# Performance work log

Hardware: AMD Instinct MI355X
Metric: run time of the kernel (lower is better)

The kernel has to match this reference:

```python
import jax, jax.numpy as jnp
import numpy as np
import math

D_MODEL = 1024
N_HEADS = 16
D_K = D_MODEL // N_HEADS
THRESH = 0.1  # attention probs below this are zeroed


def setup_inputs() -> dict:
    key = jax.random.key(0)
    ks = jax.random.split(key, 9)
    B, S, D = 2, 2048, D_MODEL
    scale = 1.0 / math.sqrt(D)
    x = jax.random.normal(ks[0], (B, S, D), dtype=jnp.float32)
    Wq = jax.random.normal(ks[1], (D, D), dtype=jnp.float32) * scale
    bq = jax.random.normal(ks[2], (D,), dtype=jnp.float32) * 0.01
    Wk = jax.random.normal(ks[3], (D, D), dtype=jnp.float32) * scale
    bk = jax.random.normal(ks[4], (D,), dtype=jnp.float32) * 0.01
    Wv = jax.random.normal(ks[5], (D, D), dtype=jnp.float32) * scale
    bv = jax.random.normal(ks[6], (D,), dtype=jnp.float32) * 0.01
    Wo = jax.random.normal(ks[7], (D, D), dtype=jnp.float32) * scale
    bo = jax.random.normal(ks[8], (D,), dtype=jnp.float32) * 0.01
    return {"x": x, "Wq": Wq, "bq": bq, "Wk": Wk, "bk": bk,
            "Wv": Wv, "bv": bv, "Wo": Wo, "bo": bo}


def _split_heads(t):
    B, S, D = t.shape
    return t.reshape(B, S, N_HEADS, D_K).transpose(0, 2, 1, 3)  # [B,H,S,dk]


def reference(x, Wq, bq, Wk, bk, Wv, bv, Wo, bo):
    # torch nn.Linear: y = x @ W.T + b
    q = _split_heads(x @ Wq.T + bq)
    k = _split_heads(x @ Wk.T + bk)
    v = _split_heads(x @ Wv.T + bv)
    scores = jnp.einsum('bhqd,bhkd->bhqk', q, k) / math.sqrt(D_K)
    probs = jax.nn.softmax(scores, axis=-1)          # full unmasked softmax (returned)
    keep = probs >= THRESH                            # ~low_attention_mask
    probs_model = jnp.where(keep, probs, 0.0)        # masked_fill; dropout is identity in eval
    ctx = jnp.einsum('bhqk,bhkd->bhqd', probs_model, v)
    B, H, S, dk = ctx.shape
    merged = ctx.transpose(0, 2, 1, 3).reshape(B, S, H * dk)
    out = merged @ Wo.T + bo
    attention_sum = probs.sum(axis=1)                # [B,S,S] sum over heads
    attention_mask = keep.astype(jnp.float32).sum(axis=1)  # [B,S,S]
    return (out, attention_sum, attention_mask)
```

## Files before the change

kernel.cpp:

```cpp
#include <hip/hip_runtime.h>

#define SDIM 2048
#define DDIM 1024
#define NH 16
#define DK 64
#define NB 2
#define MROWS (NB * SDIM)
#define MAXEV 65536
#define EXPC 0.18033688011112f
#define L01 -3.3219281f

typedef _Float16 f16x8 __attribute__((ext_vector_type(8)));
typedef _Float16 f16x4 __attribute__((ext_vector_type(4)));
typedef float f32x4 __attribute__((ext_vector_type(4)));

__device__ __forceinline__ void ld_lds16(const _Float16* g, _Float16* l) {
  __builtin_amdgcn_global_load_lds(
      (const __attribute__((address_space(1))) void*)g,
      (__attribute__((address_space(3))) void*)l, 16, 0, 0);
}

__global__ __launch_bounds__(256) void cvt_f16(
    const float* __restrict__ x, const float* __restrict__ wq,
    const float* __restrict__ wk, const float* __restrict__ wv,
    _Float16* __restrict__ xh, _Float16* __restrict__ wqh,
    _Float16* __restrict__ wkh, _Float16* __restrict__ wvh) {
  int i = blockIdx.x * 256 + threadIdx.x;
  const float* src;
  _Float16* dst;
  int off;
  if (i < 1048576) {
    src = x; dst = xh; off = i;
  } else if (i < 1310720) {
    src = wq; dst = wqh; off = i - 1048576;
  } else if (i < 1572864) {
    src = wk; dst = wkh; off = i - 1310720;
  } else {
    src = wv; dst = wvh; off = i - 1572864;
  }
  float4 v = ((const float4*)src)[off];
  f16x4 h;
  h[0] = (_Float16)v.x; h[1] = (_Float16)v.y;
  h[2] = (_Float16)v.z; h[3] = (_Float16)v.w;
  ((f16x4*)dst)[off] = h;
}

__global__ __launch_bounds__(256, 2) void proj_gemm(
    const _Float16* __restrict__ xh, const _Float16* __restrict__ Wqh,
    const _Float16* __restrict__ Wkh, const _Float16* __restrict__ Wvh,
    const float* __restrict__ bq, const float* __restrict__ bk,
    const float* __restrict__ bv, _Float16* __restrict__ Qo,
    _Float16* __restrict__ Ko, float* __restrict__ Vo) {
  __shared__ __align__(16) _Float16 SMEM[16896];
  _Float16* sA = SMEM;
  _Float16* sB = SMEM + 128 * 64;
  const int t = threadIdx.x;
  const int lane = t & 63, wv = t >> 6;
  const int lr = lane & 15, quad = lane >> 4;
  const int wm = wv >> 1, wn = wv & 1;
  const int m0 = blockIdx.y * 128, n0 = blockIdx.x * 128;
  const int z = blockIdx.z;
  const _Float16* Bp = z == 0 ? Wqh : (z == 1 ? Wkh : Wvh);
  const float* bias = z == 0 ? bq : (z == 1 ? bk : bv);

  const int strow = t >> 3;
  const int stchunk = t & 7;
  const int stsrc = (stchunk ^ (strow & 7)) * 8;

  f32x4 acc[4][4];
#pragma unroll
  for (int i = 0; i < 4; ++i)
#pragma unroll
    for (int j = 0; j < 4; ++j) acc[i][j] = (f32x4){0.f, 0.f, 0.f, 0.f};

  for (int k0 = 0; k0 < DDIM; k0 += 64) {
    __syncthreads();
#pragma unroll
    for (int i = 0; i < 4; ++i) {
      const int row = i * 32 + strow;
      ld_lds16(&xh[(size_t)(m0 + row) * DDIM + k0 + stsrc],
               &sA[row * 64 + stchunk * 8]);
      ld_lds16(&Bp[(size_t)(n0 + row) * DDIM + k0 + stsrc],
               &sB[row * 64 + stchunk * 8]);
    }
    __syncthreads();
    f16x8 af[4][2], bf[4][2];
#pragma unroll
    for (int i = 0; i < 4; ++i)
#pragma unroll
      for (int kk = 0; kk < 2; ++kk) {
        const int ph = ((kk * 4 + quad) ^ (lr & 7)) * 8;
        af[i][kk] = *(const f16x8*)&sA[(wm * 64 + i * 16 + lr) * 64 + ph];
        bf[i][kk] = *(const f16x8*)&sB[(wn * 64 + i * 16 + lr) * 64 + ph];
      }
#pragma unroll
    for (int kk = 0; kk < 2; ++kk)
#pragma unroll
      for (int i = 0; i < 4; ++i)
#pragma unroll
        for (int j = 0; j < 4; ++j)
          acc[i][j] = __builtin_amdgcn_mfma_f32_16x16x32_f16(
              af[i][kk], bf[j][kk], acc[i][j], 0, 0, 0);
  }

  const int h0 = n0 >> 6;
  const int bb = m0 >> 11;
  const int s0 = m0 & 2047;
  __syncthreads();
  if (z < 2) {
    _Float16* dst = z == 0 ? Qo : Ko;
    _Float16* Tb = SMEM;
    const float scl = z == 0 ? EXPC : 1.0f;
#pragma unroll 1
    for (int p = 0; p < 2; ++p) {
      if (wm == p) {
#pragma unroll
        for (int j = 0; j < 4; ++j) {
          const int ng = wn * 64 + j * 16 + lr;
          const float bvv = bias[n0 + ng];
#pragma unroll
          for (int i = 0; i < 4; ++i)
#pragma unroll
            for (int r = 0; r < 4; ++r) {
              const int row = i * 16 + quad * 4 + r;
              Tb[row * 136 + ng] = (_Float16)((acc[i][j][r] + bvv) * scl);
            }
        }
      }
      __syncthreads();
      const int srow = t >> 4, scc = t & 15;
#pragma unroll
      for (int ii = 0; ii < 4; ++ii) {
        const int row = ii * 16 + srow;
        const int s = s0 + p * 64 + row;
        const int h = h0 + (scc >> 3);
        const int d = (scc & 7) * 8;
        f16x8 v = *(const f16x8*)&Tb[row * 136 + scc * 8];
        *(f16x8*)&dst[((size_t)(bb * NH + h) * SDIM + s) * DK + d] = v;
      }
      __syncthreads();
    }
  } else {
    float* Tb = (float*)SMEM;
#pragma unroll 1
    for (int p = 0; p < 2; ++p) {
      if (wm == p) {
#pragma unroll
        for (int j = 0; j < 4; ++j) {
          const int ng = wn * 64 + j * 16 + lr;
          const float bvv = bias[n0 + ng];
#pragma unroll
          for (int i = 0; i < 4; ++i)
#pragma unroll
            for (int r = 0; r < 4; ++r) {
              const int row = i * 16 + quad * 4 + r;
              Tb[row * 132 + ng] = acc[i][j][r] + bvv;
            }
        }
      }
      __syncthreads();
      const int srow = t >> 5, scc = t & 31;
#pragma unroll
      for (int ii = 0; ii < 8; ++ii) {
        const int row = ii * 8 + srow;
        const int s = s0 + p * 64 + row;
        const int h = h0 + (scc >> 4);
        const int d = (scc & 15) * 4;
        float4 v = *(const float4*)&Tb[row * 132 + scc * 4];
        *(float4*)&Vo[((size_t)(bb * NH + h) * SDIM + s) * DK + d] = v;
      }
      __syncthreads();
    }
  }
}

__global__ __launch_bounds__(256, 3) void attn_denom(
    const _Float16* __restrict__ Q, const _Float16* __restrict__ K,
    float* __restrict__ laOut) {
  __shared__ __align__(16) _Float16 KS[3 * 8192];
  const int t = threadIdx.x;
  const int lane = t & 63, wave = t >> 6;
  const int quad = lane >> 4, lr = lane & 15;
  const int id = blockIdx.x;
  const int xcd = id & 7, inner = id >> 3;
  const int bh = xcd * 4 + (inner >> 5);
  const int q0 = (inner & 31) * 64;
  const _Float16* Qh = Q + (size_t)bh * SDIM * DK;
  const _Float16* Kh = K + (size_t)bh * SDIM * DK;
  const size_t qoff = (size_t)(q0 + wave * 16 + lr) * DK + quad * 8;
  const f16x8 aq0 = *(const f16x8*)&Qh[qoff];
  const f16x8 aq1 = *(const f16x8*)&Qh[qoff + 32];
  const int strow = t >> 3, stchunk = t & 7;
  const int stsrc = (stchunk ^ (strow & 7)) * 8;
  const int ph0 = (quad ^ (lr & 7)) * 8;
  const int ph1 = ((4 + quad) ^ (lr & 7)) * 8;

#define STAGE_DN(KP, BUF)                                                  \
  {                                                                        \
    _Pragma("unroll") for (int i = 0; i < 4; ++i)                          \
        ld_lds16(&(KP)[(size_t)(i * 32 + strow) * DK + stsrc],             \
                 &(BUF)[(i * 32 + strow) * 64 + stchunk * 8]);             \
  }

#define COMPUTE_DN(BUF)                                                   \
  _Pragma("unroll") for (int c = 0; c < 8; ++c) {                         \
    f16x8 b0 = *(const f16x8*)&(BUF)[(c * 16 + lr) * 64 + ph0];           \
    f16x8 b1 = *(const f16x8*)&(BUF)[(c * 16 + lr) * 64 + ph1];           \
    f32x4 acc = {0.f, 0.f, 0.f, 0.f};                                     \
    acc = __builtin_amdgcn_mfma_f32_16x16x32_f16(aq0, b0, acc, 0, 0, 0);  \
    acc = __builtin_amdgcn_mfma_f32_16x16x32_f16(aq1, b1, acc, 0, 0, 0);  \
    _Pragma("unroll") for (int r = 0; r < 4; ++r)                         \
        dsum[r] += __builtin_amdgcn_exp2f(acc[r]);                        \
  }

  float dsum[4] = {0.f, 0.f, 0.f, 0.f};
  const _Float16* kp = Kh;
  STAGE_DN(kp, KS);
  kp += 128 * DK;
  int cb = 0;
#pragma unroll 1
  for (int kt = 0; kt < 16; ++kt) {
    const int nb_ = cb == 2 ? 0 : cb + 1;
    if (kt + 1 < 16) {
      STAGE_DN(kp, KS + nb_ * 8192);
      kp += 128 * DK;
    }
    asm volatile("" ::: "memory");
    if (kt + 1 < 16)
      asm volatile("s_waitcnt vmcnt(4)" ::: "memory");
    else
      asm volatile("s_waitcnt vmcnt(0)" ::: "memory");
    __builtin_amdgcn_s_barrier();
    asm volatile("" ::: "memory");
    __builtin_amdgcn_s_setprio(1);
    COMPUTE_DN(KS + cb * 8192);
    __builtin_amdgcn_s_setprio(0);
    cb = nb_;
  }
#pragma unroll
  for (int m = 1; m < 16; m <<= 1)
#pragma unroll
    for (int r = 0; r < 4; ++r)
      dsum[r] += __shfl_xor(dsum[r], m, 64);
  if (lr == 0) {
#pragma unroll
    for (int r = 0; r < 4; ++r)
      laOut[(size_t)bh * SDIM + q0 + wave * 16 + quad * 4 + r] =
          -__builtin_amdgcn_logf(dsum[r]);
  }
#undef STAGE_DN
#undef COMPUTE_DN
}

__global__ __launch_bounds__(256, 3) void attn_pass2(
    const _Float16* __restrict__ Q, const _Float16* __restrict__ K,
    const float* __restrict__ la, float* __restrict__ attSum,
    float* __restrict__ attMask, float4* __restrict__ ev,
    int* __restrict__ ecnt) {
  __shared__ __align__(16) _Float16 KS[3 * 8192];
  float* Tbuf = (float*)KS;
  const int t = threadIdx.x;
  const int lane = t & 63, wave = t >> 6;
  const int quad = lane >> 4, lr = lane & 15;
  const int id = blockIdx.x;
  const int xcd = id & 7, inner = id >> 3;
  const int b = xcd >> 2;
  const int q0 = (((xcd >> 1) & 1) * 16 + (inner >> 4)) * 64;
  const int k0 = ((xcd & 1) * 16 + (inner & 15)) * 64;
  const int strow = t >> 3, stchunk = t & 7;
  const int stsrc = (stchunk ^ (strow & 7)) * 8;
  const int ph0 = (quad ^ (lr & 7)) * 8;
  const int ph1 = ((4 + quad) ^ (lr & 7)) * 8;

  const size_t qbase = ((size_t)(b * NH) * SDIM + q0 + wave * 16 + lr) * DK;
  const size_t dbase = (size_t)(b * NH) * SDIM + q0 + wave * 16 + quad * 4;
  const size_t hstep = (size_t)SDIM * DK;

  float asum[4][4] = {};
  float mx01 = -1e30f, mx23 = -1e30f;

  f16x8 a0c[2], a1c[2], a0n[2], a1n[2];
  float4 lavc[2], lavn[2];

#define STAGE2(KP, BUF)                                                      \
  {                                                                          \
    _Pragma("unroll") for (int hh = 0; hh < 2; ++hh) {                       \
      const _Float16* Kpp = (KP) + (size_t)hh * hstep;                       \
      _Pragma("unroll") for (int i = 0; i < 2; ++i)                          \
          ld_lds16(&Kpp[(size_t)(i * 32 + strow) * DK + stsrc],              \
                   &(BUF)[hh * 4096 + (i * 32 + strow) * 64 + stchunk * 8]); \
    }                                                                        \
  }

#define LOADQ2(QP, LAP, A0, A1, LV)                                          \
  {                                                                          \
    _Pragma("unroll") for (int hh = 0; hh < 2; ++hh) {                       \
      const _Float16* qpp = (QP) + (size_t)hh * hstep;                       \
      A0[hh] = *(const f16x8*)&qpp[quad * 8];                                \
      A1[hh] = *(const f16x8*)&qpp[32 + quad * 8];                           \
      LV[hh] = *(const float4*)&(LAP)[(size_t)hh * SDIM];                    \
    }                                                                        \
  }

#define COMPUTE2(BUF, A0, A1, LV)                                            \
  _Pragma("unroll") for (int hh = 0; hh < 2; ++hh) {                         \
    const _Float16* Ksh = &(BUF)[hh * 4096];                                 \
    const f32x4 cinit = {LV[hh].x, LV[hh].y, LV[hh].z, LV[hh].w};            \
    _Pragma("unroll") for (int c = 0; c < 4; ++c) {                          \
      f16x8 b0 = *(const f16x8*)&Ksh[(c * 16 + lr) * 64 + ph0];              \
      f16x8 b1 = *(const f16x8*)&Ksh[(c * 16 + lr) * 64 + ph1];              \
      f32x4 acc = cinit;                  \
      acc = __builtin_amdgcn_mfma_f32_16x16x32_f16(A0[hh], b0, acc, 0, 0, 0);\
      acc = __builtin_amdgcn_mfma_f32_16x16x32_f16(A1[hh], b1, acc, 0, 0, 0);\
      mx01 = fmaxf(fmaxf(acc[0], acc[1]), mx01);                 \
      mx23 = fmaxf(fmaxf(acc[2], acc[3]), mx23);                             \
      asum[c][0] += __builtin_amdgcn_exp2f(acc[0]);                          \
      asum[c][1] += __builtin_amdgcn_exp2f(acc[1]);                          \
      asum[c][2] += __builtin_amdgcn_exp2f(acc[2]);                          \
      asum[c][3] += __builtin_amdgcn_exp2f(acc[3]);                          \
    }                                                                        \
  }

  const _Float16* kp = K + (size_t)(b * NH) * hstep + (size_t)k0 * DK;
  const _Float16* qp = Q + qbase;
  const float* lap = la + dbase;
  STAGE2(kp, KS);
  LOADQ2(qp, lap, a0c, a1c, lavc);
  kp += 2 * hstep; qp += 2 * hstep; lap += 2 * SDIM;
  int cb = 0;
#pragma unroll 1
  for (int s = 0; s < 8; ++s) {
    const int nb_ = cb == 2 ? 0 : cb + 1;
    if (s + 1 < 8) {
      STAGE2(kp, KS + nb_ * 8192);
      LOADQ2(qp, lap, a0n, a1n, lavn);
      kp += 2 * hstep; qp += 2 * hstep; lap += 2 * SDIM;
    }
    asm volatile("" ::: "memory");
    if (s + 1 < 8)
      asm volatile("s_waitcnt vmcnt(10)" ::: "memory");
    else
      asm volatile("s_waitcnt vmcnt(0)" ::: "memory");
    __builtin_amdgcn_s_barrier();
    asm volatile("" ::: "memory");
    __builtin_amdgcn_s_setprio(1);
    COMPUTE2(KS + cb * 8192, a0c, a1c, lavc);
    __builtin_amdgcn_s_setprio(0);
    if (s + 1 < 8) {
#pragma unroll
      for (int hh = 0; hh < 2; ++hh) {
        a0c[hh] = a0n[hh]; a1c[hh] = a1n[hh]; lavc[hh] = lavn[hh];
      }
    }
    cb = nb_;
  }
#undef STAGE2
#undef LOADQ2
#undef COMPUTE2

  const float mx = fmaxf(mx01, mx23);
  if (__any(mx >= L01)) {
    float amask[4][4] = {};
#pragma unroll 1
    for (int h = 0; h < NH; ++h) {
      const _Float16* Kp =
          K + (size_t)(b * NH + h) * hstep + (size_t)k0 * DK;
      const size_t ho = (size_t)h * hstep;
      const f16x8 aq0 = *(const f16x8*)&Q[qbase + ho + quad * 8];
      const f16x8 aq1 = *(const f16x8*)&Q[qbase + ho + 32 + quad * 8];
      const float4 l4 = *(const float4*)&la[dbase + (size_t)h * SDIM];
      const float lar[4] = {l4.x, l4.y, l4.z, l4.w};
#pragma unroll 1
      for (int c = 0; c < 4; ++c) {
        const f16x8 b0 = *(const f16x8*)&Kp[(c * 16 + lr) * DK + quad * 8];
        const f16x8 b1 = *(const f16x8*)&Kp[(c * 16 + lr) * DK + 32 + quad * 8];
        f32x4 acc = {0.f, 0.f, 0.f, 0.f};
        acc = __builtin_amdgcn_mfma_f32_16x16x32_f16(aq0, b0, acc, 0, 0, 0);
        acc = __builtin_amdgcn_mfma_f32_16x16x32_f16(aq1, b1, acc, 0, 0, 0);
#pragma unroll 1
        for (int r = 0; r < 4; ++r) {
          const float p = __builtin_amdgcn_exp2f(acc[r] + lar[r]);
          if (p >= 0.1f) {
            amask[c][r] += 1.0f;
            int idx = atomicAdd(ecnt, 1);
            if (idx < MAXEV)
              ev[idx] = make_float4(
                  __int_as_float(b * NH + h),
                  __int_as_float(q0 + wave * 16 + quad * 4 + r),
                  __int_as_float(k0 + c * 16 + lr), p);
          }
        }
      }
    }
#pragma unroll
    for (int c = 0; c < 4; ++c)
#pragma unroll
      for (int r = 0; r < 4; ++r)
        if (amask[c][r] != 0.0f) {
          const size_t row = (size_t)(b * SDIM) + q0 + wave * 16 + quad * 4 + r;
          attMask[row * SDIM + k0 + c * 16 + lr] = amask[c][r];
        }
  }
  const int g8 = t >> 3;
  const int l8 = (t & 7) * 4;
  __syncthreads();
#pragma unroll
  for (int c = 0; c < 4; ++c)
#pragma unroll
    for (int r = 0; r < 4; ++r)
      Tbuf[(wave * 16 + quad * 4 + r) * 68 + c * 16 + lr] = asum[c][r];
  __syncthreads();
#pragma unroll
  for (int p = 0; p < 2; ++p)
#pragma unroll
    for (int qh = 0; qh < 2; ++qh) {
      const int row = p * 32 + g8, col = qh * 32 + l8;
      f32x4 v = *(const f32x4*)&Tbuf[row * 68 + col];
      __builtin_nontemporal_store(
          v, (f32x4*)&attSum[((size_t)(b * SDIM) + q0 + row) * SDIM + k0 + col]);
    }
}

__global__ __launch_bounds__(64) void apply_events(
    const float4* __restrict__ ev, const int* __restrict__ ecnt,
    const float* __restrict__ V, float* __restrict__ merged,
    int* __restrict__ flags) {
  int n = *ecnt;
  if (n > MAXEV) n = MAXEV;
  const int d = threadIdx.x;
  for (int e = blockIdx.x; e < n; e += gridDim.x) {
    float4 r = ev[e];
    int bh = __float_as_int(r.x);
    int q = __float_as_int(r.y);
    int kc = __float_as_int(r.z);
    float p = r.w;
    int b = bh >> 4, h = bh & 15;
    atomicAdd(&merged[((size_t)(b * SDIM + q)) * DDIM + h * DK + d],
              p * V[((size_t)bh * SDIM + kc) * DK + d]);
    if (d == 0) flags[b * SDIM + q] = 1;
  }
}

__global__ __launch_bounds__(256) void out_gemm(const float* __restrict__ A,
                                                const float* __restrict__ W,
                                                const float* __restrict__ bias,
                                                float* __restrict__ out,
                                                const int* __restrict__ flags) {
  __shared__ float As[16][68];
  __shared__ float Ws[16][68];
  __shared__ int anyF;
  const int t = threadIdx.x;
  const int tx = t & 15, ty = t >> 4;
  const int m0 = blockIdx.y * 64;
  const int n0 = blockIdx.x * 64;
  if (t == 0) anyF = 0;
  __syncthreads();
  if (t < 64 && flags[m0 + t]) anyF = 1;
  __syncthreads();
  const int nb = n0 + tx * 4;
  const float4 bv = *(const float4*)&bias[nb];
  if (!anyF) {
#pragma unroll
    for (int r = 0; r < 4; ++r)
      *(float4*)&out[(size_t)(m0 + ty * 4 + r) * DDIM + nb] = bv;
    return;
  }
  const int lr = t >> 2;
  const int lc = (t & 3) * 4;
  float acc[4][4] = {};
  for (int k0 = 0; k0 < DDIM; k0 += 16) {
    __syncthreads();
    float4 av = *(const float4*)&A[(size_t)(m0 + lr) * DDIM + k0 + lc];
    float4 wv = *(const float4*)&W[(size_t)(n0 + lr) * DDIM + k0 + lc];
    As[lc + 0][lr] = av.x; As[lc + 1][lr] = av.y;
    As[lc + 2][lr] = av.z; As[lc + 3][lr] = av.w;
    Ws[lc + 0][lr] = wv.x; Ws[lc + 1][lr] = wv.y;
    Ws[lc + 2][lr] = wv.z; Ws[lc + 3][lr] = wv.w;
    __syncthreads();
#pragma unroll
    for (int kk = 0; kk < 16; ++kk) {
      float4 a4 = *(const float4*)&As[kk][ty * 4];
      float4 b4 = *(const float4*)&Ws[kk][tx * 4];
      const float a[4] = {a4.x, a4.y, a4.z, a4.w};
      const float b[4] = {b4.x, b4.y, b4.z, b4.w};
#pragma unroll
      for (int r = 0; r < 4; ++r)
#pragma unroll
        for (int c = 0; c < 4; ++c)
          acc[r][c] = fmaf(a[r], b[c], acc[r][c]);
    }
  }
#pragma unroll
  for (int r = 0; r < 4; ++r) {
    float4 o;
    o.x = acc[r][0] + bv.x;
    o.y = acc[r][1] + bv.y;
    o.z = acc[r][2] + bv.z;
    o.w = acc[r][3] + bv.w;
    *(float4*)&out[(size_t)(m0 + ty * 4 + r) * DDIM + nb] = o;
  }
}

extern "C" void kernel_launch(void* const* d_in, const int* in_sizes, int n_in,
                              void* d_out, int out_size, void* d_ws,
                              size_t ws_size, hipStream_t stream) {
  const float* x = (const float*)d_in[0];
  const float* Wq = (const float*)d_in[1];
  const float* bq = (const float*)d_in[2];
  const float* Wk = (const float*)d_in[3];
  const float* bk = (const float*)d_in[4];
  const float* Wv = (const float*)d_in[5];
  const float* bv = (const float*)d_in[6];
  const float* Wo = (const float*)d_in[7];
  const float* bo = (const float*)d_in[8];

  float* out = (float*)d_out;
  float* attSum = out + (size_t)MROWS * DDIM;
  float* attMask = attSum + (size_t)NB * SDIM * SDIM;

  char* ws = (char*)d_ws;
  const size_t bigF = (size_t)MROWS * DDIM * sizeof(float);
  const size_t bigH = (size_t)MROWS * DDIM * sizeof(_Float16);
  const size_t wH = (size_t)DDIM * DDIM * sizeof(_Float16);
  float* merged = (float*)ws;    ws += bigF;
  int* flags = (int*)ws;         ws += (size_t)MROWS * sizeof(int);
  int* ecnt = (int*)ws;          ws += 16;
  const size_t zeroSpan = bigF + (size_t)MROWS * sizeof(int) + 16;
  _Float16* Qh = (_Float16*)ws;  ws += bigH;
  _Float16* Kh = (_Float16*)ws;  ws += bigH;
  float* V = (float*)ws;         ws += bigF;
  _Float16* xh = (_Float16*)ws;  ws += bigH;
  _Float16* Wqh = (_Float16*)ws; ws += wH;
  _Float16* Wkh = (_Float16*)ws; ws += wH;
  _Float16* Wvh = (_Float16*)ws; ws += wH;
  float* laBuf = (float*)ws;     ws += (size_t)NB * NH * SDIM * sizeof(float);
  float4* ev = (float4*)ws;      ws += (size_t)MAXEV * sizeof(float4);

  hipMemsetAsync(merged, 0, zeroSpan, stream);
  hipMemsetAsync(attMask, 0, (size_t)NB * SDIM * SDIM * sizeof(float), stream);

  dim3 blk(256);
  cvt_f16<<<dim3(7168), blk, 0, stream>>>(x, Wq, Wk, Wv, xh, Wqh, Wkh, Wvh);
  proj_gemm<<<dim3(8, 32, 3), blk, 0, stream>>>(xh, Wqh, Wkh, Wvh, bq, bk, bv,
                                                Qh, Kh, V);
  attn_denom<<<dim3(1024), blk, 0, stream>>>(Qh, Kh, laBuf);
  attn_pass2<<<dim3(2048), blk, 0, stream>>>(Qh, Kh, laBuf, attSum,
                                             attMask, ev, ecnt);
  apply_events<<<dim3(256), dim3(64), 0, stream>>>(ev, ecnt, V, merged, flags);
  out_gemm<<<dim3(16, 64), blk, 0, stream>>>(merged, Wo, bo, out, flags);
}
```

Before: 244.6 us.

## Pipeline attn_pass2 per head with 4-slot LDS ring to raise occupancy

The score-sum pass now stages one head's K tile per step into a 4-slot ring buffer with prefetch distance two, instead of two heads per step in a 3-slot buffer. This cuts LDS use from 48KB to 32KB and the register footprint of the Q/la prefetch, so launch bounds go from 3 to 4 blocks per CU. The cost is twice as many barrier-separated steps, each doing less work, and tighter hand-written vmcnt accounting. The smaller LDS array is also shared with a later Tbuf scratch, which must still fit.

```diff
diff --git a/kernel.cpp b/kernel.cpp
--- a/kernel.cpp
+++ b/kernel.cpp
@@ -252,12 +252,12 @@
 #undef COMPUTE_DN
 }
 
-__global__ __launch_bounds__(256, 3) void attn_pass2(
+__global__ __launch_bounds__(256, 4) void attn_pass2(
     const _Float16* __restrict__ Q, const _Float16* __restrict__ K,
     const float* __restrict__ la, float* __restrict__ attSum,
     float* __restrict__ attMask, float4* __restrict__ ev,
     int* __restrict__ ecnt) {
-  __shared__ __align__(16) _Float16 KS[3 * 8192];
+  __shared__ __align__(16) _Float16 KS[4 * 4096];
   float* Tbuf = (float*)KS;
   const int t = threadIdx.x;
   const int lane = t & 63, wave = t >> 6;
@@ -279,39 +279,32 @@
   float asum[4][4] = {};
   float mx01 = -1e30f, mx23 = -1e30f;
 
-  f16x8 a0c[2], a1c[2], a0n[2], a1n[2];
-  float4 lavc[2], lavn[2];
-
-#define STAGE2(KP, BUF)                                                      \
+  f16x8 a0c, a1c, a0n, a1n;
+  float4 lavc, lavn;
+
+#define STAGE1(KP, BUF)                                                      \
   {                                                                          \
-    _Pragma("unroll") for (int hh = 0; hh < 2; ++hh) {                       \
-      const _Float16* Kpp = (KP) + (size_t)hh * hstep;                       \
-      _Pragma("unroll") for (int i = 0; i < 2; ++i)                          \
-          ld_lds16(&Kpp[(size_t)(i * 32 + strow) * DK + stsrc],              \
-                   &(BUF)[hh * 4096 + (i * 32 + strow) * 64 + stchunk * 8]); \
-    }                                                                        \
-  }
-
-#define LOADQ2(QP, LAP, A0, A1, LV)                                          \
+    _Pragma("unroll") for (int i = 0; i < 2; ++i)                            \
+        ld_lds16(&(KP)[(size_t)(i * 32 + strow) * DK + stsrc],               \
+                 &(BUF)[(i * 32 + strow) * 64 + stchunk * 8]);               \
+  }
+
+#define LOADQ1(QP, LAP, A0, A1, LV)                                          \
   {                                                                          \
-    _Pragma("unroll") for (int hh = 0; hh < 2; ++hh) {                       \
-      const _Float16* qpp = (QP) + (size_t)hh * hstep;                       \
-      A0[hh] = *(const f16x8*)&qpp[quad * 8];                                \
-      A1[hh] = *(const f16x8*)&qpp[32 + quad * 8];                           \
-      LV[hh] = *(const float4*)&(LAP)[(size_t)hh * SDIM];                    \
-    }                                                                        \
-  }
-
-#define COMPUTE2(BUF, A0, A1, LV)                                            \
-  _Pragma("unroll") for (int hh = 0; hh < 2; ++hh) {                         \
-    const _Float16* Ksh = &(BUF)[hh * 4096];                                 \
-    const f32x4 cinit = {LV[hh].x, LV[hh].y, LV[hh].z, LV[hh].w};            \
+    A0 = *(const f16x8*)&(QP)[quad * 8];                                     \
+    A1 = *(const f16x8*)&(QP)[32 + quad * 8];                                \
+    LV = *(const float4*)(LAP);                                              \
+  }
+
+#define COMPUTE1(BUF, A0, A1, LV)                                            \
+  {                                                                          \
+    const f32x4 cinit = {LV.x, LV.y, LV.z, LV.w};                            \
     _Pragma("unroll") for (int c = 0; c < 4; ++c) {                          \
-      f16x8 b0 = *(const f16x8*)&Ksh[(c * 16 + lr) * 64 + ph0];              \
-      f16x8 b1 = *(const f16x8*)&Ksh[(c * 16 + lr) * 64 + ph1];              \
+      f16x8 b0 = *(const f16x8*)&(BUF)[(c * 16 + lr) * 64 + ph0];            \
+      f16x8 b1 = *(const f16x8*)&(BUF)[(c * 16 + lr) * 64 + ph1];            \
       f32x4 acc = cinit;                  \
-      acc = __builtin_amdgcn_mfma_f32_16x16x32_f16(A0[hh], b0, acc, 0, 0, 0);\
-      acc = __builtin_amdgcn_mfma_f32_16x16x32_f16(A1[hh], b1, acc, 0, 0, 0);\
+      acc = __builtin_amdgcn_mfma_f32_16x16x32_f16(A0, b0, acc, 0, 0, 0);    \
+      acc = __builtin_amdgcn_mfma_f32_16x16x32_f16(A1, b1, acc, 0, 0, 0);    \
       mx01 = fmaxf(fmaxf(acc[0], acc[1]), mx01);                 \
       mx23 = fmaxf(fmaxf(acc[2], acc[3]), mx23);                             \
       asum[c][0] += __builtin_amdgcn_exp2f(acc[0]);                          \
@@ -324,39 +317,41 @@
   const _Float16* kp = K + (size_t)(b * NH) * hstep + (size_t)k0 * DK;
   const _Float16* qp = Q + qbase;
   const float* lap = la + dbase;
-  STAGE2(kp, KS);
-  LOADQ2(qp, lap, a0c, a1c, lavc);
-  kp += 2 * hstep; qp += 2 * hstep; lap += 2 * SDIM;
+  STAGE1(kp, KS);
+  kp += hstep;
+  STAGE1(kp, KS + 4096);
+  kp += hstep;
+  LOADQ1(qp, lap, a0c, a1c, lavc);
+  qp += hstep; lap += SDIM;
   int cb = 0;
 #pragma unroll 1
-  for (int s = 0; s < 8; ++s) {
-    const int nb_ = cb == 2 ? 0 : cb + 1;
-    if (s + 1 < 8) {
-      STAGE2(kp, KS + nb_ * 8192);
-      LOADQ2(qp, lap, a0n, a1n, lavn);
-      kp += 2 * hstep; qp += 2 * hstep; lap += 2 * SDIM;
+  for (int h = 0; h < NH; ++h) {
+    if (h + 2 < NH) {
+      STAGE1(kp, KS + ((cb + 2) & 3) * 4096);
+      kp += hstep;
+    }
+    if (h + 1 < NH) {
+      LOADQ1(qp, lap, a0n, a1n, lavn);
+      qp += hstep; lap += SDIM;
     }
     asm volatile("" ::: "memory");
-    if (s + 1 < 8)
+    if (h == NH - 1)
+      asm volatile("s_waitcnt vmcnt(6)" ::: "memory");
+    else
       asm volatile("s_waitcnt vmcnt(10)" ::: "memory");
-    else
-      asm volatile("s_waitcnt vmcnt(0)" ::: "memory");
     __builtin_amdgcn_s_barrier();
     asm volatile("" ::: "memory");
     __builtin_amdgcn_s_setprio(1);
-    COMPUTE2(KS + cb * 8192, a0c, a1c, lavc);
+    COMPUTE1(KS + cb * 4096, a0c, a1c, lavc);
     __builtin_amdgcn_s_setprio(0);
-    if (s + 1 < 8) {
-#pragma unroll
-      for (int hh = 0; hh < 2; ++hh) {
-        a0c[hh] = a0n[hh]; a1c[hh] = a1n[hh]; lavc[hh] = lavn[hh];
-      }
-    }
-    cb = nb_;
-  }
-#undef STAGE2
-#undef LOADQ2
-#undef COMPUTE2
+    if (h + 1 < NH) {
+      a0c = a0n; a1c = a1n; lavc = lavn;
+    }
+    cb = (cb + 1) & 3;
+  }
+#undef STAGE1
+#undef LOADQ1
+#undef COMPUTE1
 
   const float mx = fmaxf(mx01, mx23);
   if (__any(mx >= L01)) {
```

After: 246.5 us. Within noise of the previous version (+0.8%).
